# Kernel optimization log

Hardware: AMD Instinct MI355X
Metric: run time of the kernel (lower is better)

The kernel has to match this reference:

```python
import jax, jax.numpy as jnp
import numpy as np


def setup_inputs() -> dict:
    key = jax.random.key(0)
    k1, k2, k3, k4 = jax.random.split(key, 4)
    B, S, K, N, G = 4, 2048, 4096, 11008, 128
    x = jax.random.normal(k1, (B, S, K), dtype=jnp.float16)
    # each int holds two packed 4-bit weights (low nibble = even k, high nibble = odd k)
    weight_packed = jax.random.randint(k2, (K // 2, N), 0, 256, dtype=jnp.int32)
    # small positive group-wise scales (typical magnitude for int4 quant)
    scales = (jax.random.uniform(k3, (K // G, N), dtype=jnp.float32) * 0.01 + 0.001).astype(jnp.float16)
    bias = jax.random.normal(k4, (N,), dtype=jnp.float16)
    return {"x": x, "weight_packed": weight_packed, "scales": scales,
            "bias": bias, "group_size": G}


def _dequant(weight_packed, scales, group_size):
    # weight_packed: [K//2, N] ints in [0,255]; two 4-bit codes per entry.
    low = weight_packed & 0xF           # even k indices
    high = (weight_packed >> 4) & 0xF   # odd k indices
    # interleave along K: [K//2, 2, N] -> [K, N]
    wq = jnp.stack([low, high], axis=1).reshape(-1, weight_packed.shape[1])
    # per-group scale: group g covers rows [g*group_size, (g+1)*group_size)
    s_full = jnp.repeat(scales, group_size, axis=0)  # [K, N]
    return (wq.astype(jnp.float16) - jnp.float16(8)) * s_full


def reference(x, weight_packed, scales, bias, group_size):
    w = _dequant(weight_packed, scales, group_size)          # [K, N] fp16
    out = jnp.einsum('bsk,kn->bsn', x, w)                    # fp16 GEMM
    return out + bias
```

## Files before the change

kernel.cpp:

```cpp
#include <hip/hip_runtime.h>

typedef unsigned short u16;
typedef unsigned int   u32;
typedef _Float16       f16;
typedef f16   f16x2  __attribute__((ext_vector_type(2)));
typedef f16   f16x8  __attribute__((ext_vector_type(8)));
typedef float f32x4  __attribute__((ext_vector_type(4)));
typedef u32   u32x2  __attribute__((ext_vector_type(2)));
typedef u32   u32x4  __attribute__((ext_vector_type(4)));

#define MDIM 8192
#define KDIM 4096
#define NDIM 11008
#define NKT  64

#define X16_BYTES  67108864ull
#define W16_BYTES  90177536ull
#define WS_NEEDED  (X16_BYTES + W16_BYTES)

typedef const __attribute__((address_space(1))) u32 gu32;
typedef __attribute__((address_space(3)))       u32 su32;

__global__ __launch_bounds__(256) void cvt_x(const float* __restrict__ x, u16* __restrict__ x16)
{
    const size_t i = ((size_t)blockIdx.x * 256 + threadIdx.x) * 8;
    f32x4 a = *(const f32x4*)(x + i);
    f32x4 b = *(const f32x4*)(x + i + 4);
    u32x4 v;
    v.x = __builtin_bit_cast(u32, __builtin_amdgcn_cvt_pkrtz(a[0], a[1]));
    v.y = __builtin_bit_cast(u32, __builtin_amdgcn_cvt_pkrtz(a[2], a[3]));
    v.z = __builtin_bit_cast(u32, __builtin_amdgcn_cvt_pkrtz(b[0], b[1]));
    v.w = __builtin_bit_cast(u32, __builtin_amdgcn_cvt_pkrtz(b[2], b[3]));
    *(u32x4*)(x16 + i) = v;
}

__global__ __launch_bounds__(256) void dq_w(const int* __restrict__ wpk,
                                            const float* __restrict__ sc,
                                            u16* __restrict__ w16)
{
    const int kb = blockIdx.x / 43;
    const int n  = (blockIdx.x % 43) * 256 + threadIdx.x;
    const f16 sh = (f16)sc[(kb >> 4) * NDIM + n];
    const f16x2 s2 = {sh, sh};
    const f16x2 cm = {(f16)(-1032.0f), (f16)(-1032.0f)};
    u32 wds[4];
#pragma unroll
    for (int j = 0; j < 4; ++j) {
        const u32 w = (u32)wpk[(size_t)(kb * 4 + j) * NDIM + n];
        const u32 hb = 0x64006400u | (w & 15u) | ((w & 0xF0u) << 12);
        const f16x2 rr = (__builtin_bit_cast(f16x2, hb) + cm) * s2;
        wds[j] = __builtin_bit_cast(u32, rr);
    }
    u32x4 v = {wds[0], wds[1], wds[2], wds[3]};
    *(u32x4*)(w16 + ((size_t)kb * NDIM + n) * 8) = v;
}

__global__ __launch_bounds__(256, 4) void gemm_f16(
    const u16* __restrict__ x16,
    const u16* __restrict__ w16,
    const float* __restrict__ bias,
    float*       __restrict__ out)
{
    __shared__ __align__(16) u16 ldsA[128 * 64];
    __shared__ __align__(16) u16 ldsB[64 * 128];

    const int tid  = threadIdx.x;
    const int wave = tid >> 6;
    const int lane = tid & 63;
    const int wm   = wave >> 1;
    const int wn   = wave & 1;
    const int quad = lane >> 4;
    const int l15  = lane & 15;

    const int bid   = blockIdx.y * 86 + blockIdx.x;
    const int swz   = (bid & 7) * 688 + (bid >> 3);
    const int n_blk = swz % 86;
    const int m_blk = swz / 86;
    const int m0    = m_blk * 128;
    const int n0    = n_blk * 128;

    f32x4 acc[4][4];
    const f32x4 zero4 = {0.f, 0.f, 0.f, 0.f};
#pragma unroll
    for (int mt = 0; mt < 4; ++mt)
#pragma unroll
        for (int nt = 0; nt < 4; ++nt) acc[mt][nt] = zero4;

    const u16* aglb[4];
    const u16* bglb[4];
#pragma unroll
    for (int p = 0; p < 4; ++p) {
        const int c   = p * 256 + tid;
        const int row = c >> 3;
        const int kcl = c & 7;
        const int kc  = kcl ^ (row & 7);
        aglb[p] = x16 + (size_t)(m0 + row) * KDIM + kc * 8;
        const int kbl = c >> 7;
        const int nl  = c & 127;
        bglb[p] = w16 + ((size_t)kbl * NDIM + n0 + nl) * 8;
    }
    u16* adst = ldsA + tid * 8;
    u16* bdst = ldsB + tid * 8;

    for (int kt = 0; kt < NKT; ++kt) {
#pragma unroll
        for (int p = 0; p < 4; ++p)
            __builtin_amdgcn_global_load_lds((gu32*)(const void*)(aglb[p] + kt * 64),
                                             (su32*)(void*)(adst + p * 2048), 16, 0, 0);
#pragma unroll
        for (int p = 0; p < 4; ++p)
            __builtin_amdgcn_global_load_lds((gu32*)(const void*)(bglb[p] + (size_t)kt * NDIM * 64),
                                             (su32*)(void*)(bdst + p * 2048), 16, 0, 0);

        __syncthreads();

#pragma unroll
        for (int ks = 0; ks < 2; ++ks) {
            f16x8 af[4], bfr[4];
#pragma unroll
            for (int mt = 0; mt < 4; ++mt) {
                const int mrow = wm * 64 + mt * 16 + l15;
                const int kcl  = (ks * 4 + quad) ^ (mrow & 7);
                af[mt] = *(const f16x8*)&ldsA[(mrow * 8 + kcl) * 8];
            }
#pragma unroll
            for (int nt = 0; nt < 4; ++nt)
                bfr[nt] = *(const f16x8*)&ldsB[((ks * 4 + quad) * 128 + wn * 64 + nt * 16 + l15) * 8];
#pragma unroll
            for (int mt = 0; mt < 4; ++mt)
#pragma unroll
                for (int nt = 0; nt < 4; ++nt)
                    acc[mt][nt] = __builtin_amdgcn_mfma_f32_16x16x32_f16(
                        af[mt], bfr[nt], acc[mt][nt], 0, 0, 0);
        }

        __syncthreads();
    }

    float bv[4];
#pragma unroll
    for (int nt = 0; nt < 4; ++nt)
        bv[nt] = bias[n0 + wn * 64 + nt * 16 + l15];
#pragma unroll
    for (int mt = 0; mt < 4; ++mt) {
        const int row = m0 + wm * 64 + mt * 16 + quad * 4;
#pragma unroll
        for (int nt = 0; nt < 4; ++nt) {
            const int col = n0 + wn * 64 + nt * 16 + l15;
#pragma unroll
            for (int r = 0; r < 4; ++r)
                out[(size_t)(row + r) * NDIM + col] = acc[mt][nt][r] + bv[nt];
        }
    }
}

#define LDA  72
#define ABUF (128 * LDA)
#define BBUF 8192

__global__ __launch_bounds__(256) void int4_gemm_fb(
    const float* __restrict__ x, const int* __restrict__ wpk,
    const float* __restrict__ sc, const float* __restrict__ bias, float* __restrict__ out)
{
    __shared__ __align__(16) u16 ldsA[2 * ABUF];
    __shared__ __align__(16) u16 ldsB[2 * BBUF];

    const int tid  = threadIdx.x;
    const int wave = tid >> 6;
    const int lane = tid & 63;
    const int wm   = wave >> 1;
    const int wn   = wave & 1;
    const int quad = lane >> 4;
    const int l15  = lane & 15;
    const int bid   = blockIdx.y * 86 + blockIdx.x;
    const int swz   = (bid & 7) * 688 + (bid >> 3);
    const int n_blk = swz % 86;
    const int m_blk = swz / 86;
    const int m0    = m_blk * 128;
    const int n0    = n_blk * 128;
    const int n_local = tid & 127;
    const int half    = tid >> 7;
    const int gn      = n0 + n_local;

    f32x4 acc[4][4];
    const f32x4 zero4 = {0.f, 0.f, 0.f, 0.f};
#pragma unroll
    for (int mt = 0; mt < 4; ++mt)
#pragma unroll
        for (int nt = 0; nt < 4; ++nt) acc[mt][nt] = zero4;

    f32x4 areg[8];
    int   pw[16];
    float scur;
#pragma unroll
    for (int p = 0; p < 8; ++p) {
        const int c = p * 256 + tid;
        areg[p] = *(const f32x4*)(x + (size_t)(m0 + (c >> 4)) * KDIM + (c & 15) * 4);
    }
#pragma unroll
    for (int i = 0; i < 16; ++i) pw[i] = wpk[(half * 16 + i) * NDIM + gn];
    scur = sc[gn];
    {
        const f16 sh = (f16)scur;
        const f16x2 s2 = {sh, sh};
        const f16x2 cm = {(f16)(-1032.0f), (f16)(-1032.0f)};
#pragma unroll
        for (int q = 0; q < 4; ++q) {
            u32 wds[4];
#pragma unroll
            for (int r = 0; r < 4; ++r) {
                const u32 w = (u32)pw[q * 4 + r];
                const u32 hb = 0x64006400u | (w & 15u) | ((w & 0xF0u) << 12);
                const f16x2 rr = (__builtin_bit_cast(f16x2, hb) + cm) * s2;
                wds[r] = __builtin_bit_cast(u32, rr);
            }
            u32x4 wv = {wds[0], wds[1], wds[2], wds[3]};
            *(u32x4*)&ldsB[(half * 512 + q * 128 + n_local) * 8] = wv;
        }
#pragma unroll
        for (int p = 0; p < 8; ++p) {
            const int c = p * 256 + tid;
            u32x2 v;
            v.x = __builtin_bit_cast(u32, __builtin_amdgcn_cvt_pkrtz(areg[p][0], areg[p][1]));
            v.y = __builtin_bit_cast(u32, __builtin_amdgcn_cvt_pkrtz(areg[p][2], areg[p][3]));
            *(u32x2*)&ldsA[(c >> 4) * LDA + (c & 15) * 4] = v;
        }
    }
#pragma unroll
    for (int p = 0; p < 8; ++p) {
        const int c = p * 256 + tid;
        areg[p] = *(const f32x4*)(x + (size_t)(m0 + (c >> 4)) * KDIM + 64 + (c & 15) * 4);
    }
#pragma unroll
    for (int i = 0; i < 16; ++i) pw[i] = wpk[(32 + half * 16 + i) * NDIM + gn];
    scur = sc[gn];
    __syncthreads();

    for (int kt = 0; kt < NKT; ++kt) {
        const int cur = kt & 1;
        const u16* asrc = ldsA + cur * ABUF;
        const u16* bsrc = ldsB + cur * BBUF;
        if (kt + 1 < NKT) {
            u16* adst = ldsA + (cur ^ 1) * ABUF;
            u16* bdst = ldsB + (cur ^ 1) * BBUF;
            const f16 sh = (f16)scur;
            const f16x2 s2 = {sh, sh};
            const f16x2 cm = {(f16)(-1032.0f), (f16)(-1032.0f)};
#pragma unroll
            for (int q = 0; q < 4; ++q) {
                u32 wds[4];
#pragma unroll
                for (int r = 0; r < 4; ++r) {
                    const u32 w = (u32)pw[q * 4 + r];
                    const u32 hb = 0x64006400u | (w & 15u) | ((w & 0xF0u) << 12);
                    const f16x2 rr = (__builtin_bit_cast(f16x2, hb) + cm) * s2;
                    wds[r] = __builtin_bit_cast(u32, rr);
                }
                u32x4 wv = {wds[0], wds[1], wds[2], wds[3]};
                *(u32x4*)&bdst[(half * 512 + q * 128 + n_local) * 8] = wv;
            }
#pragma unroll
            for (int p = 0; p < 8; ++p) {
                const int c = p * 256 + tid;
                u32x2 v;
                v.x = __builtin_bit_cast(u32, __builtin_amdgcn_cvt_pkrtz(areg[p][0], areg[p][1]));
                v.y = __builtin_bit_cast(u32, __builtin_amdgcn_cvt_pkrtz(areg[p][2], areg[p][3]));
                *(u32x2*)&adst[(c >> 4) * LDA + (c & 15) * 4] = v;
            }
            if (kt + 2 < NKT) {
#pragma unroll
                for (int p = 0; p < 8; ++p) {
                    const int c = p * 256 + tid;
                    areg[p] = *(const f32x4*)(x + (size_t)(m0 + (c >> 4)) * KDIM
                                                + (kt + 2) * 64 + (c & 15) * 4);
                }
                const int kp0 = (kt + 2) * 32 + half * 16;
#pragma unroll
                for (int i = 0; i < 16; ++i) pw[i] = wpk[(kp0 + i) * NDIM + gn];
                scur = sc[((kt + 2) >> 1) * NDIM + gn];
            }
        }
#pragma unroll
        for (int ks = 0; ks < 2; ++ks) {
            f16x8 af[4], bfr[4];
#pragma unroll
            for (int mt = 0; mt < 4; ++mt)
                af[mt] = *(const f16x8*)&asrc[(wm * 64 + mt * 16 + l15) * LDA + ks * 32 + quad * 8];
#pragma unroll
            for (int nt = 0; nt < 4; ++nt)
                bfr[nt] = *(const f16x8*)&bsrc[(ks * 512 + quad * 128 + wn * 64 + nt * 16 + l15) * 8];
#pragma unroll
            for (int mt = 0; mt < 4; ++mt)
#pragma unroll
                for (int nt = 0; nt < 4; ++nt)
                    acc[mt][nt] = __builtin_amdgcn_mfma_f32_16x16x32_f16(
                        af[mt], bfr[nt], acc[mt][nt], 0, 0, 0);
        }
        if (kt + 1 < NKT) __syncthreads();
    }

    float bv[4];
#pragma unroll
    for (int nt = 0; nt < 4; ++nt)
        bv[nt] = bias[n0 + wn * 64 + nt * 16 + l15];
#pragma unroll
    for (int mt = 0; mt < 4; ++mt) {
        const int row = m0 + wm * 64 + mt * 16 + quad * 4;
#pragma unroll
        for (int nt = 0; nt < 4; ++nt) {
            const int col = n0 + wn * 64 + nt * 16 + l15;
#pragma unroll
            for (int r = 0; r < 4; ++r)
                out[(size_t)(row + r) * NDIM + col] = acc[mt][nt][r] + bv[nt];
        }
    }
}

extern "C" void kernel_launch(void* const* d_in, const int* in_sizes, int n_in,
                              void* d_out, int out_size, void* d_ws, size_t ws_size,
                              hipStream_t stream) {
    const float* x    = (const float*)d_in[0];
    const int*   wpk  = (const int*)d_in[1];
    const float* scl  = (const float*)d_in[2];
    const float* bias = (const float*)d_in[3];

    if (d_ws != nullptr && ws_size >= WS_NEEDED) {
        u16* x16 = (u16*)d_ws;
        u16* w16 = (u16*)((char*)d_ws + X16_BYTES);
        cvt_x<<<dim3(16384), dim3(256), 0, stream>>>(x, x16);
        dq_w <<<dim3(22016), dim3(256), 0, stream>>>(wpk, scl, w16);
        dim3 grid(NDIM / 128, MDIM / 128);
        gemm_f16<<<grid, dim3(256), 0, stream>>>(x16, w16, bias, (float*)d_out);
    } else {
        dim3 grid(NDIM / 128, MDIM / 128);
        int4_gemm_fb<<<grid, dim3(256), 0, stream>>>(x, wpk, scl, bias, (float*)d_out);
    }
}
```

Measured before the change: 1.348 ms.

## Replace fp16 GEMM with 256x256 tile, 8-wave, double-buffered phased pipeline

Replaces the 128x128, 4-wave GEMM with a 256x256 tile run by 512 threads in a single 128KB LDS buffer split into two stages. Global-to-LDS loads for the next k-tiles are issued between groups of MFMAs, with explicit vmcnt waits, barriers, sched_barrier and setprio. The goal is to hide load latency behind compute and raise arithmetic intensity per byte loaded. In exchange it uses far more LDS and registers per block (two blocks per CU at most). The hand-tuned waitcnt sequencing is fragile, and 43 n-tiles by 32 m-tiles gives a grid that may balance poorly across CUs.

Measured after the change: 1.103 ms. 18.2% less time.

```diff
diff --git a/kernel.cpp b/kernel.cpp
--- a/kernel.cpp
+++ b/kernel.cpp
@@ -55,95 +55,144 @@
     *(u32x4*)(w16 + ((size_t)kb * NDIM + n) * 8) = v;
 }
 
-__global__ __launch_bounds__(256, 4) void gemm_f16(
+__global__ __launch_bounds__(512, 2) void gemm_8ph(
     const u16* __restrict__ x16,
     const u16* __restrict__ w16,
     const float* __restrict__ bias,
     float*       __restrict__ out)
 {
-    __shared__ __align__(16) u16 ldsA[128 * 64];
-    __shared__ __align__(16) u16 ldsB[64 * 128];
+    __shared__ __align__(16) u16 lds[65536];
 
     const int tid  = threadIdx.x;
     const int wave = tid >> 6;
     const int lane = tid & 63;
-    const int wm   = wave >> 1;
-    const int wn   = wave & 1;
+    const int wm   = wave >> 2;
+    const int wn   = wave & 3;
     const int quad = lane >> 4;
     const int l15  = lane & 15;
-
-    const int bid   = blockIdx.y * 86 + blockIdx.x;
-    const int swz   = (bid & 7) * 688 + (bid >> 3);
-    const int n_blk = swz % 86;
-    const int m_blk = swz / 86;
-    const int m0    = m_blk * 128;
-    const int n0    = n_blk * 128;
-
-    f32x4 acc[4][4];
+    const int l7   = l15 & 7;
+
+    const int bid   = blockIdx.y * 43 + blockIdx.x;
+    const int swz   = (bid & 7) * 172 + (bid >> 3);
+    const int n_blk = swz % 43;
+    const int m_blk = swz / 43;
+    const int m0    = m_blk * 256;
+    const int n0    = n_blk * 256;
+
+    u32 offA[2], offB[2];
+#pragma unroll
+    for (int p = 0; p < 2; ++p) {
+        const int c    = p * 512 + tid;
+        const int rowh = c >> 3;
+        const int slot = c & 7;
+        const int kc   = slot ^ (rowh & 7);
+        offA[p] = (u32)rowh * KDIM + (u32)kc * 8;
+        offB[p] = (u32)(c >> 8) * (NDIM * 8) + (u32)(n0 + (c & 255)) * 8;
+    }
+    const u16* xb = x16 + (size_t)m0 * KDIM;
+
+    const u32 aBase0 = (u32)(wm * 16 + l15) * 64;
+    const u32 sl0    = (u32)((quad)     ^ l7) * 8;
+    const u32 sl1    = (u32)((quad + 4) ^ l7) * 8;
+    const u32 bBase0 = 16384u + (u32)quad * 2048u + (u32)(wn * 64 + l15) * 8;
+
+    f32x4 acc[8][4];
     const f32x4 zero4 = {0.f, 0.f, 0.f, 0.f};
 #pragma unroll
-    for (int mt = 0; mt < 4; ++mt)
+    for (int mt = 0; mt < 8; ++mt)
 #pragma unroll
         for (int nt = 0; nt < 4; ++nt) acc[mt][nt] = zero4;
 
-    const u16* aglb[4];
-    const u16* bglb[4];
-#pragma unroll
-    for (int p = 0; p < 4; ++p) {
-        const int c   = p * 256 + tid;
-        const int row = c >> 3;
-        const int kcl = c & 7;
-        const int kc  = kcl ^ (row & 7);
-        aglb[p] = x16 + (size_t)(m0 + row) * KDIM + kc * 8;
-        const int kbl = c >> 7;
-        const int nl  = c & 127;
-        bglb[p] = w16 + ((size_t)kbl * NDIM + n0 + nl) * 8;
-    }
-    u16* adst = ldsA + tid * 8;
-    u16* bdst = ldsB + tid * 8;
-
-    for (int kt = 0; kt < NKT; ++kt) {
-#pragma unroll
-        for (int p = 0; p < 4; ++p)
-            __builtin_amdgcn_global_load_lds((gu32*)(const void*)(aglb[p] + kt * 64),
-                                             (su32*)(void*)(adst + p * 2048), 16, 0, 0);
-#pragma unroll
-        for (int p = 0; p < 4; ++p)
-            __builtin_amdgcn_global_load_lds((gu32*)(const void*)(bglb[p] + (size_t)kt * NDIM * 64),
-                                             (su32*)(void*)(bdst + p * 2048), 16, 0, 0);
-
-        __syncthreads();
-
-#pragma unroll
-        for (int ks = 0; ks < 2; ++ks) {
-            f16x8 af[4], bfr[4];
-#pragma unroll
-            for (int mt = 0; mt < 4; ++mt) {
-                const int mrow = wm * 64 + mt * 16 + l15;
-                const int kcl  = (ks * 4 + quad) ^ (mrow & 7);
-                af[mt] = *(const f16x8*)&ldsA[(mrow * 8 + kcl) * 8];
-            }
-#pragma unroll
-            for (int nt = 0; nt < 4; ++nt)
-                bfr[nt] = *(const f16x8*)&ldsB[((ks * 4 + quad) * 128 + wn * 64 + nt * 16 + l15) * 8];
-#pragma unroll
-            for (int mt = 0; mt < 4; ++mt)
-#pragma unroll
-                for (int nt = 0; nt < 4; ++nt)
-                    acc[mt][nt] = __builtin_amdgcn_mfma_f32_16x16x32_f16(
-                        af[mt], bfr[nt], acc[mt][nt], 0, 0, 0);
-        }
-
-        __syncthreads();
-    }
+#define GLD(SRC, DSTIDX)                                                       \
+    __builtin_amdgcn_global_load_lds((gu32*)(const void*)(SRC),                \
+                                     (su32*)(void*)(&lds[(DSTIDX)]), 16, 0, 0)
+
+#define STAGE_A(KT, H, DD) do {                                                \
+    GLD(xb + (size_t)(KT) * 64 + (H) * (128 * KDIM) + offA[0],                 \
+        (u32)(DD) * 32768u + ((u32)(H) * 1024u + (u32)tid) * 8u);              \
+    GLD(xb + (size_t)(KT) * 64 + (H) * (128 * KDIM) + offA[1],                 \
+        (u32)(DD) * 32768u + ((u32)(H) * 1024u + 512u + (u32)tid) * 8u);       \
+} while (0)
+
+#define STAGE_B(KT, H, DD) do {                                                \
+    GLD(w16 + (size_t)(KT) * (NDIM * 64) + (size_t)(H) * (NDIM * 32) + offB[0],\
+        (u32)(DD) * 32768u + 16384u + ((u32)(H) * 1024u + (u32)tid) * 8u);     \
+    GLD(w16 + (size_t)(KT) * (NDIM * 64) + (size_t)(H) * (NDIM * 32) + offB[1],\
+        (u32)(DD) * 32768u + 16384u + ((u32)(H) * 1024u + 512u + (u32)tid) * 8u); \
+} while (0)
+
+#define DS_A(DD, MT, SL) (*(const f16x8*)&lds[(DD) * 32768u + aBase0 + (MT) * 2048u + (SL)])
+#define DS_B(DD, KS, NT) (*(const f16x8*)&lds[(DD) * 32768u + bBase0 + (KS) * 8192u + (NT) * 128u])
+
+#define MM8(MT, AK0, AK1)                                                                 \
+    acc[MT][0] = __builtin_amdgcn_mfma_f32_16x16x32_f16(AK0, b00, acc[MT][0], 0, 0, 0);   \
+    acc[MT][1] = __builtin_amdgcn_mfma_f32_16x16x32_f16(AK0, b01, acc[MT][1], 0, 0, 0);   \
+    acc[MT][2] = __builtin_amdgcn_mfma_f32_16x16x32_f16(AK0, b02, acc[MT][2], 0, 0, 0);   \
+    acc[MT][3] = __builtin_amdgcn_mfma_f32_16x16x32_f16(AK0, b03, acc[MT][3], 0, 0, 0);   \
+    acc[MT][0] = __builtin_amdgcn_mfma_f32_16x16x32_f16(AK1, b10, acc[MT][0], 0, 0, 0);   \
+    acc[MT][1] = __builtin_amdgcn_mfma_f32_16x16x32_f16(AK1, b11, acc[MT][1], 0, 0, 0);   \
+    acc[MT][2] = __builtin_amdgcn_mfma_f32_16x16x32_f16(AK1, b12, acc[MT][2], 0, 0, 0);   \
+    acc[MT][3] = __builtin_amdgcn_mfma_f32_16x16x32_f16(AK1, b13, acc[MT][3], 0, 0, 0);
+
+#define PH_IN()  __builtin_amdgcn_sched_barrier(0);                            \
+                 __builtin_amdgcn_s_barrier();                                 \
+                 asm volatile("s_waitcnt lgkmcnt(0)" ::: "memory");            \
+                 __builtin_amdgcn_sched_barrier(0);                            \
+                 __builtin_amdgcn_s_setprio(1)
+
+#define PH_OUT() __builtin_amdgcn_s_setprio(0);                                \
+                 __builtin_amdgcn_sched_barrier(0);                            \
+                 __builtin_amdgcn_s_barrier()
+
+#define GROUP(T, D, EA1, ET2, VMTOK) do {                                      \
+                                         \
+    f16x8 b00 = DS_B(D,0,0), b01 = DS_B(D,0,1), b02 = DS_B(D,0,2), b03 = DS_B(D,0,3); \
+    f16x8 b10 = DS_B(D,1,0), b11 = DS_B(D,1,1), b12 = DS_B(D,1,2), b13 = DS_B(D,1,3); \
+    f16x8 aa0 = DS_A(D,0,sl0), aa1 = DS_A(D,0,sl1);                            \
+    f16x8 ab0 = DS_A(D,1,sl0), ab1 = DS_A(D,1,sl1);                            \
+    if (EA1) STAGE_A((T) + 1, 1, (D) ^ 1);                                     \
+    PH_IN(); MM8(0, aa0, aa1) MM8(1, ab0, ab1) PH_OUT();                       \
+                                                         \
+    aa0 = DS_A(D,2,sl0); aa1 = DS_A(D,2,sl1);                                  \
+    ab0 = DS_A(D,3,sl0); ab1 = DS_A(D,3,sl1);                                  \
+    if (ET2) STAGE_B((T) + 2, 0, (D));                                         \
+    PH_IN(); MM8(2, aa0, aa1) MM8(3, ab0, ab1) PH_OUT();                       \
+                                                         \
+    aa0 = DS_A(D,4,sl0); aa1 = DS_A(D,4,sl1);                                  \
+    ab0 = DS_A(D,5,sl0); ab1 = DS_A(D,5,sl1);                                  \
+    if (ET2) STAGE_B((T) + 2, 1, (D));                                         \
+    PH_IN(); MM8(4, aa0, aa1) MM8(5, ab0, ab1) PH_OUT();                       \
+                                                         \
+    aa0 = DS_A(D,6,sl0); aa1 = DS_A(D,6,sl1);                                  \
+    ab0 = DS_A(D,7,sl0); ab1 = DS_A(D,7,sl1);                                  \
+    if (ET2) STAGE_A((T) + 2, 0, (D));                                         \
+    PH_IN(); MM8(6, aa0, aa1) MM8(7, ab0, ab1)                                 \
+    __builtin_amdgcn_s_setprio(0);                                             \
+    __builtin_amdgcn_sched_barrier(0);                                         \
+    asm volatile("s_waitcnt " VMTOK ::: "memory");                             \
+    __builtin_amdgcn_s_barrier();                                              \
+} while (0)
+
+    STAGE_A(0, 0, 0); STAGE_A(0, 1, 0); STAGE_B(0, 0, 0); STAGE_B(0, 1, 0);
+    STAGE_B(1, 0, 1); STAGE_B(1, 1, 1); STAGE_A(1, 0, 1);
+    asm volatile("s_waitcnt vmcnt(6)" ::: "memory");
+    __builtin_amdgcn_s_barrier();
+
+#pragma unroll 1
+    for (int t = 0; t < NKT - 2; t += 2) {
+        GROUP(t,     0, 1, 1, "vmcnt(6)");
+        GROUP(t + 1, 1, 1, 1, "vmcnt(6)");
+    }
+    GROUP(NKT - 2, 0, 1, 0, "vmcnt(0)");
+    GROUP(NKT - 1, 1, 0, 0, "vmcnt(0)");
 
     float bv[4];
 #pragma unroll
     for (int nt = 0; nt < 4; ++nt)
         bv[nt] = bias[n0 + wn * 64 + nt * 16 + l15];
 #pragma unroll
-    for (int mt = 0; mt < 4; ++mt) {
-        const int row = m0 + wm * 64 + mt * 16 + quad * 4;
+    for (int mt = 0; mt < 8; ++mt) {
+        const int row = m0 + mt * 32 + wm * 16 + quad * 4;
 #pragma unroll
         for (int nt = 0; nt < 4; ++nt) {
             const int col = n0 + wn * 64 + nt * 16 + l15;
@@ -152,6 +201,15 @@
                 out[(size_t)(row + r) * NDIM + col] = acc[mt][nt][r] + bv[nt];
         }
     }
+#undef GLD
+#undef STAGE_A
+#undef STAGE_B
+#undef DS_A
+#undef DS_B
+#undef MM8
+#undef PH_IN
+#undef PH_OUT
+#undef GROUP
 }
 
 #define LDA  72
@@ -329,8 +387,8 @@
         u16* w16 = (u16*)((char*)d_ws + X16_BYTES);
         cvt_x<<<dim3(16384), dim3(256), 0, stream>>>(x, x16);
         dq_w <<<dim3(22016), dim3(256), 0, stream>>>(wpk, scl, w16);
-        dim3 grid(NDIM / 128, MDIM / 128);
-        gemm_f16<<<grid, dim3(256), 0, stream>>>(x16, w16, bias, (float*)d_out);
+        dim3 grid(NDIM / 256, MDIM / 256);
+        gemm_8ph<<<grid, dim3(512), 0, stream>>>(x16, w16, bias, (float*)d_out);
     } else {
         dim3 grid(NDIM / 128, MDIM / 128);
         int4_gemm_fb<<<grid, dim3(256), 0, stream>>>(x, wpk, scl, bias, (float*)d_out);
```
